# Performance work log

Hardware: AMD Instinct MI355X
Metric: run time of the kernel (lower is better)

Reference implementation:

```python
import jax, jax.numpy as jnp
import numpy as np

N_NODES = 100000
N_EDGES = 1600000
HID = 128
HEADS = 8
DK = HID // HEADS
N_LAYERS = 4
IN_DIM = 32
N_CLASSES = 16


def _ln(x, g, b, eps=1e-5):
    mu = x.mean(-1, keepdims=True)
    var = x.var(-1, keepdims=True)
    return (x - mu) / jnp.sqrt(var + eps) * g + b


def setup_inputs() -> dict:
    key = jax.random.key(0)
    ks = jax.random.split(key, 24)
    s = 0.05
    inp = {
        'feat': jax.random.randint(ks[0], (N_NODES,), 0, IN_DIM, dtype=jnp.int32),
        'edge_src': jax.random.randint(ks[1], (N_EDGES,), 0, N_NODES, dtype=jnp.int32),
        'edge_dst': jnp.sort(jax.random.randint(ks[2], (N_EDGES,), 0, N_NODES, dtype=jnp.int32)),
        'emb': jax.random.normal(ks[3], (IN_DIM, HID), jnp.float32) * s,
        'Wq': jax.random.normal(ks[4], (N_LAYERS, HID, HID), jnp.float32) * s,
        'Wk': jax.random.normal(ks[5], (N_LAYERS, HID, HID), jnp.float32) * s,
        'Wv': jax.random.normal(ks[6], (N_LAYERS, HID, HID), jnp.float32) * s,
        'Wo': jax.random.normal(ks[7], (N_LAYERS, HID, HID), jnp.float32) * s,
        'bo': jnp.zeros((N_LAYERS, HID), jnp.float32),
        'ln1_g': jnp.ones((N_LAYERS, HID), jnp.float32),
        'ln1_b': jnp.zeros((N_LAYERS, HID), jnp.float32),
        'W1': jax.random.normal(ks[8], (N_LAYERS, HID, 2 * HID), jnp.float32) * s,
        'b1': jnp.zeros((N_LAYERS, 2 * HID), jnp.float32),
        'W2': jax.random.normal(ks[9], (N_LAYERS, 2 * HID, HID), jnp.float32) * s,
        'b2': jnp.zeros((N_LAYERS, HID), jnp.float32),
        'ln2_g': jnp.ones((N_LAYERS, HID), jnp.float32),
        'ln2_b': jnp.zeros((N_LAYERS, HID), jnp.float32),
        'mW0': jax.random.normal(ks[10], (HID, HID // 2), jnp.float32) * s,
        'mb0': jnp.zeros((HID // 2,), jnp.float32),
        'mW1': jax.random.normal(ks[11], (HID // 2, HID // 4), jnp.float32) * s,
        'mb1': jnp.zeros((HID // 4,), jnp.float32),
        'mW2': jax.random.normal(ks[12], (HID // 4, N_CLASSES), jnp.float32) * s,
        'mb2': jnp.zeros((N_CLASSES,), jnp.float32),
    }
    return inp


def reference(feat, edge_src, edge_dst, emb, Wq, Wk, Wv, Wo, bo, ln1_g, ln1_b,
              W1, b1, W2, b2, ln2_g, ln2_b, mW0, mb0, mW1, mb1, mW2, mb2):
    N = feat.shape[0]
    h = emb[feat]  # [N, HID] embedding gather
    inv_sqrt_dk = jnp.float32(1.0 / np.sqrt(DK))
    for l in range(Wq.shape[0]):
        h_in1 = h
        q = (h @ Wq[l]).reshape(N, HEADS, DK)
        k = (h @ Wk[l]).reshape(N, HEADS, DK)
        v = (h @ Wv[l]).reshape(N, HEADS, DK)
        # per-edge scores: K[src] . Q[dst], scaled, clipped, exponentiated
        sc = jnp.einsum('ehd,ehd->eh', k[edge_src], q[edge_dst]) * inv_sqrt_dk
        sc = jnp.exp(jnp.clip(sc, -5.0, 5.0))  # [E, HEADS]
        wV = jax.ops.segment_sum(sc[:, :, None] * v[edge_src], edge_dst, num_segments=N)
        z = jax.ops.segment_sum(sc, edge_dst, num_segments=N)
        attn = (wV / (z[:, :, None] + 1e-6)).reshape(N, HID)
        h = h_in1 + (attn @ Wo[l] + bo[l])  # residual + O proj
        h = _ln(h, ln1_g[l], ln1_b[l])
        h_in2 = h
        f = jax.nn.relu(h @ W1[l] + b1[l]) @ W2[l] + b2[l]
        h = _ln(h_in2 + f, ln2_g[l], ln2_b[l])
    # MLPReadout: HID -> HID/2 -> HID/4 -> n_classes
    h = jax.nn.relu(h @ mW0 + mb0)
    h = jax.nn.relu(h @ mW1 + mb1)
    return h @ mW2 + mb2
```

## Files before the change

kernel.cpp:

```cpp
#include <hip/hip_runtime.h>
#include <hip/hip_fp16.h>

#define HID 128
#define N_LAYERS 4
#define IN_DIM 32
#define N_CLASSES 16

typedef _Float16 f16x8 __attribute__((ext_vector_type(8)));
typedef float f32x2 __attribute__((ext_vector_type(2)));
typedef __attribute__((ext_vector_type(4))) float f32x4;
typedef unsigned int uint_t;

#if defined(__has_builtin)
#if __has_builtin(__builtin_amdgcn_cvt_pk_f32_fp8)
#define HAVE_CVT_FP8 1
#endif
#if __has_builtin(__builtin_amdgcn_cvt_pk_fp8_f32)
#define HAVE_ENC_FP8 1
#endif
#endif

__device__ __forceinline__ unsigned short f2bf(float f) {
    unsigned int u = __float_as_uint(f);
    return (unsigned short)((u + 0x7FFFu + ((u >> 16) & 1u)) >> 16);
}
__device__ __forceinline__ float2 up16(uint_t u) {
    __half2 h = *(__half2*)&u;
    return __half22float2(h);
}

__device__ __forceinline__ unsigned char f2e4m3(float f) {
    unsigned int u = __float_as_uint(f);
    unsigned char s = (unsigned char)((u >> 24) & 0x80u);
    unsigned int a = u & 0x7FFFFFFFu;
    if (a >= 0x43E00000u) return s | 0x7Eu;
    int exp = (int)(a >> 23) - 127;
    if (exp < -6) {
        int m = (int)rintf(__uint_as_float(a) * 512.f);
        return s | (unsigned char)m;
    }
    unsigned int lsb = (a >> 20) & 1u;
    a += 0x7FFFFu + lsb;
    int e8 = ((int)(a >> 23) - 127) + 7;
    unsigned int m8 = (a >> 20) & 7u;
    return s | (unsigned char)((e8 << 3) | (int)m8);
}
__device__ __forceinline__ float e4m32f(unsigned int b) {
    unsigned int s = (b & 0x80u) << 24;
    unsigned int E = (b >> 3) & 15u, m = b & 7u;
    if (E == 0) {
        float v = (float)m * 0.001953125f;
        return __uint_as_float(__float_as_uint(v) | s);
    }
    return __uint_as_float(s | ((E + 120u) << 23) | (m << 20));
}
__device__ __forceinline__ unsigned char enc8(float v) {
#ifdef HAVE_ENC_FP8
    int r = __builtin_amdgcn_cvt_pk_fp8_f32(v, v, 0, false);
    return (unsigned char)(r & 0xFF);
#else
    return f2e4m3(v);
#endif
}
__device__ __forceinline__ void dec8v(uint_t u, f32x2* o) {
#ifdef HAVE_CVT_FP8
    o[0] = __builtin_amdgcn_cvt_pk_f32_fp8(u, false);
    o[1] = __builtin_amdgcn_cvt_pk_f32_fp8(u, true);
#else
    o[0] = (f32x2){e4m32f(u & 255u), e4m32f((u >> 8) & 255u)};
    o[1] = (f32x2){e4m32f((u >> 16) & 255u), e4m32f(u >> 24)};
#endif
}

__global__ void detect_kernel(const unsigned int* __restrict__ ln1g, int* __restrict__ flag) {
    if (threadIdx.x == 0 && blockIdx.x == 0)
        *flag = (ln1g[0] == 0x3F800000u) ? 0 : 1;
}

#define NSM 11
struct SArgs {
    const void* src[NSM];
    float*      dst[NSM];
    int         cnt[NSM];
};

__global__ void conv_kernel(SArgs args, const int* __restrict__ flag) {
    int p = blockIdx.y;
    int n = args.cnt[p];
    int base = (blockIdx.x * 256 + threadIdx.x) * 4;
    if (base >= n) return;
    float* dst = args.dst[p];
    if (*flag) {
        const unsigned short* s = (const unsigned short*)args.src[p];
        #pragma unroll
        for (int j = 0; j < 4; ++j)
            dst[base + j] = __uint_as_float(((unsigned int)s[base + j]) << 16);
    } else {
        const float* s = (const float*)args.src[p];
        *(float4*)&dst[base] = *(const float4*)&s[base];
    }
}

#define NW 27
struct WArgs {
    const void* src[NW];
    int         soff[NW];
    _Float16*   dst[NW];
    int         K[NW];
    int         M[NW];
};

__global__ void wconv_kernel(WArgs a, const int* __restrict__ flag) {
    int p = blockIdx.y;
    int K = a.K[p], M = a.M[p];
    int idx = blockIdx.x * 256 + threadIdx.x;
    if (idx >= K * M) return;
    int k = idx / M, m = idx % M;
    float v;
    if (*flag)
        v = __uint_as_float(((unsigned int)((const unsigned short*)a.src[p])[a.soff[p] + idx]) << 16);
    else
        v = ((const float*)a.src[p])[a.soff[p] + idx];
    a.dst[p][(size_t)m * K + k] = (_Float16)v;
}

__global__ void csr_kernel(const int* __restrict__ dst, int* __restrict__ row_start,
                           int N, int E) {
    int n = blockIdx.x * 256 + threadIdx.x;
    if (n > N) return;
    int lo = 0, hi = E;
    while (lo < hi) {
        int mid = (lo + hi) >> 1;
        if (dst[mid] < n) lo = mid + 1; else hi = mid;
    }
    row_start[n] = lo;
}

__global__ void embed_kernel(const int* __restrict__ feat, const float* __restrict__ emb,
                             _Float16* __restrict__ h, int N) {
    int idx = blockIdx.x * 256 + threadIdx.x;
    if (idx >= N * 16) return;
    int n  = idx >> 4;
    int c8 = idx & 15;
    int f = feat[n];
    const float* s = &emb[(size_t)f * HID + c8 * 8];
    float4 a = *(const float4*)s;
    float4 b = *(const float4*)(s + 4);
    f16x8 o;
    o[0] = (_Float16)a.x; o[1] = (_Float16)a.y; o[2] = (_Float16)a.z; o[3] = (_Float16)a.w;
    o[4] = (_Float16)b.x; o[5] = (_Float16)b.y; o[6] = (_Float16)b.z; o[7] = (_Float16)b.w;
    *(f16x8*)&h[(size_t)n * HID + c8 * 8] = o;
}

template<int K, int KC, int MC>
__launch_bounds__(256)
__global__ void mfma_gemm_qkv(const _Float16* __restrict__ Ain,
                              const _Float16* __restrict__ Bt,
                              _Float16* __restrict__ q16, unsigned char* __restrict__ kvp8) {
    constexpr int NT  = MC / 16;
    constexpr int SAB = KC * 2 + 16;

    __shared__ __align__(16) char As[64 * SAB];
    __shared__ __align__(16) char Bs[MC * SAB];

    const int t    = threadIdx.x;
    const int w    = t >> 6;
    const int l    = t & 63;
    const int quad = l >> 4;
    const int lc   = l & 15;
    const int row0 = blockIdx.x * 64;
    const int mbase = blockIdx.y * MC;

    f32x4 acc[NT];
    #pragma unroll
    for (int i = 0; i < NT; ++i) acc[i] = (f32x4){0.f, 0.f, 0.f, 0.f};

    {
        constexpr int AU = 64 * KC / 8;
        #pragma unroll
        for (int i = 0; i < (AU + 255) / 256; ++i) {
            int idx = t + i * 256;
            if ((AU % 256 == 0) || idx < AU) {
                int r = idx / (KC / 8), u = idx % (KC / 8);
                *(uint4*)&As[r * SAB + u * 16] =
                    *(const uint4*)(Ain + (size_t)(row0 + r) * K + u * 8);
            }
        }
        constexpr int BU = MC * KC / 8;
        #pragma unroll
        for (int i = 0; i < (BU + 255) / 256; ++i) {
            int idx = t + i * 256;
            if ((BU % 256 == 0) || idx < BU) {
                int m = idx / (KC / 8), u = idx % (KC / 8);
                *(uint4*)&Bs[m * SAB + u * 16] =
                    *(const uint4*)(Bt + (size_t)(mbase + m) * K + u * 8);
            }
        }
        __syncthreads();
        #pragma unroll
        for (int kk = 0; kk < KC / 32; ++kk) {
            f16x8 af = *(const f16x8*)&As[(w * 16 + lc) * SAB + kk * 64 + quad * 16];
            #pragma unroll
            for (int i = 0; i < NT; ++i) {
                f16x8 bf = *(const f16x8*)&Bs[(i * 16 + lc) * SAB + kk * 64 + quad * 16];
                acc[i] = __builtin_amdgcn_mfma_f32_16x16x32_f16(af, bf, acc[i], 0, 0, 0);
            }
        }
    }

    #pragma unroll
    for (int r = 0; r < 4; ++r) {
        int row = row0 + w * 16 + quad * 4 + r;
        #pragma unroll
        for (int i = 0; i < NT; ++i) {
            float v = acc[i][r];
            int gc = mbase + i * 16 + lc;
            if (gc < 128)      q16[(size_t)row * 128 + gc] = (_Float16)v;
            else if (gc < 256) kvp8[(size_t)row * 256 + (gc - 128)] = enc8(v);
            else               kvp8[(size_t)row * 256 + 128 + (gc - 256)] = enc8(v);
        }
    }
}

template<int NEXTM, bool RMODE>
__launch_bounds__(256)
__global__ void layer_tail_fused(const _Float16* __restrict__ t2, _Float16* __restrict__ h,
                                 const _Float16* __restrict__ Wo, const _Float16* __restrict__ W1,
                                 const _Float16* __restrict__ W2,
                                 const _Float16* __restrict__ Wn, const float* __restrict__ bn,
                                 const float* __restrict__ bo,  const float* __restrict__ l1g,
                                 const float* __restrict__ l1b, const float* __restrict__ b1,
                                 const float* __restrict__ b2,  const float* __restrict__ l2g,
                                 const float* __restrict__ l2b,
                                 _Float16* __restrict__ q16, unsigned char* __restrict__ kvp8) {
    constexpr int SAB = 272;
    __shared__ __align__(16) char bufA[64 * SAB];
    __shared__ __align__(16) char bufH[64 * SAB];
    __shared__ __align__(16) char bufB[64 * SAB];

    const int t = threadIdx.x, w = t >> 6, l = t & 63;
    const int quad = l >> 4, lc = l & 15;
    const int row0 = blockIdx.x * 64;
    const int arow = (w * 16 + lc) * SAB;

    _Float16 resv[4][8];
    #pragma unroll
    for (int r = 0; r < 4; ++r) {
        int row = row0 + w * 16 + quad * 4 + r;
        #pragma unroll
        for (int j = 0; j < 8; ++j)
            resv[r][j] = h[(size_t)row * 128 + j * 16 + lc];
    }

    #pragma unroll
    for (int i = 0; i < 4; ++i) {
        int idx = t + i * 256;
        int r = idx >> 4, u = idx & 15;
        *(uint4*)&bufA[r * SAB + u * 16] = *(const uint4*)(t2 + (size_t)(row0 + r) * 128 + u * 8);
    }

    auto stageW = [&](const _Float16* src, int rowStride) {
        __syncthreads();
        #pragma unroll
        for (int i = 0; i < 4; ++i) {
            int idx = t + i * 256;
            int r = idx >> 4, u = idx & 15;
            *(uint4*)&bufB[r * SAB + u * 16] =
                *(const uint4*)(src + (size_t)r * rowStride + u * 8);
        }
        __syncthreads();
    };
    auto mf4 = [&](const char* Ar, f32x4* acc) {
        #pragma unroll
        for (int kk = 0; kk < 4; ++kk) {
            f16x8 af = *(const f16x8*)(Ar + kk * 64 + quad * 16);
            #pragma unroll
            for (int i = 0; i < 4; ++i) {
                f16x8 bf = *(const f16x8*)&bufB[(i * 16 + lc) * SAB + kk * 64 + quad * 16];
                acc[i] = __builtin_amdgcn_mfma_f32_16x16x32_f16(af, bf, acc[i], 0, 0, 0);
            }
        }
    };

    f32x4 acc[8];
    #pragma unroll
    for (int i = 0; i < 8; ++i) acc[i] = (f32x4){0.f, 0.f, 0.f, 0.f};
    #pragma unroll
    for (int c = 0; c < 2; ++c) {
        stageW(Wo + (size_t)c * 64 * 128, 128);
        mf4(bufA + arow, acc + c * 4);
    }

    {
        float gv[8], bv[8], bb[8];
        #pragma unroll
        for (int j = 0; j < 8; ++j) {
            int col = j * 16 + lc;
            gv[j] = l1g[col]; bv[j] = l1b[col]; bb[j] = bo[col];
        }
        #pragma unroll
        for (int r = 0; r < 4; ++r) {
            int lrow = (w * 16 + quad * 4 + r) * SAB;
            float v[8];
            float s = 0.f, ss = 0.f;
            #pragma unroll
            for (int j = 0; j < 8; ++j) {
                v[j] = acc[j][r] + bb[j] + (float)resv[r][j];
                s += v[j]; ss += v[j] * v[j];
            }
            #pragma unroll
            for (int m = 1; m <= 8; m <<= 1) { s += __shfl_xor(s, m); ss += __shfl_xor(ss, m); }
            float mu   = s * (1.f / 128.f);
            float rstd = rsqrtf(ss * (1.f / 128.f) - mu * mu + 1e-5f);
            #pragma unroll
            for (int j = 0; j < 8; ++j) {
                float o = (v[j] - mu) * rstd * gv[j] + bv[j];
                *(_Float16*)&bufH[lrow + (j * 16 + lc) * 2] = (_Float16)o;
            }
        }
    }

    f32x4 acc3[8];
    #pragma unroll
    for (int i = 0; i < 8; ++i) acc3[i] = (f32x4){0.f, 0.f, 0.f, 0.f};
    #pragma unroll
    for (int half = 0; half < 2; ++half) {
        #pragma unroll
        for (int c2 = 0; c2 < 2; ++c2) {
            int c = half * 2 + c2;
            stageW(W1 + (size_t)c * 64 * 128, 128);
            f32x4 a2[4];
            #pragma unroll
            for (int i = 0; i < 4; ++i) a2[i] = (f32x4){0.f, 0.f, 0.f, 0.f};
            mf4(bufH + arow, a2);
            #pragma unroll
            for (int r = 0; r < 4; ++r) {
                int lrow = (w * 16 + quad * 4 + r) * SAB;
                #pragma unroll
                for (int i = 0; i < 4; ++i) {
                    float v = a2[i][r] + b1[c * 64 + i * 16 + lc];
                    v = fmaxf(v, 0.f);
                    *(_Float16*)&bufA[lrow + c2 * 128 + (i * 16 + lc) * 2] = (_Float16)v;
                }
            }
        }
        #pragma unroll
        for (int cc = 0; cc < 2; ++cc) {
            stageW(W2 + (size_t)cc * 64 * 256 + half * 128, 256);
            mf4(bufA + arow, acc3 + cc * 4);
        }
    }

    {
        float gv[8], bv[8], bb[8];
        #pragma unroll
        for (int j = 0; j < 8; ++j) {
            int col = j * 16 + lc;
            gv[j] = l2g[col]; bv[j] = l2b[col]; bb[j] = b2[col];
        }
        #pragma unroll
        for (int r = 0; r < 4; ++r) {
            int row = row0 + w * 16 + quad * 4 + r;
            int lrow = (w * 16 + quad * 4 + r) * SAB;
            float v[8];
            float s = 0.f, ss = 0.f;
            #pragma unroll
            for (int j = 0; j < 8; ++j) {
                float res = (float)*(const _Float16*)&bufH[lrow + (j * 16 + lc) * 2];
                v[j] = acc3[j][r] + bb[j] + res;
                s += v[j]; ss += v[j] * v[j];
            }
            #pragma unroll
            for (int m = 1; m <= 8; m <<= 1) { s += __shfl_xor(s, m); ss += __shfl_xor(ss, m); }
            float mu   = s * (1.f / 128.f);
            float rstd = rsqrtf(ss * (1.f / 128.f) - mu * mu + 1e-5f);
            #pragma unroll
            for (int j = 0; j < 8; ++j) {
                float o = (v[j] - mu) * rstd * gv[j] + bv[j];
                h[(size_t)row * 128 + j * 16 + lc] = (_Float16)o;
                *(_Float16*)&bufA[lrow + (j * 16 + lc) * 2] = (_Float16)o;
            }
        }
    }

    #pragma unroll
    for (int c = 0; c < NEXTM / 64; ++c) {
        stageW(Wn + (size_t)c * 64 * 128, 128);
        f32x4 a4[4];
        #pragma unroll
        for (int i = 0; i < 4; ++i) a4[i] = (f32x4){0.f, 0.f, 0.f, 0.f};
        mf4(bufA + arow, a4);
        #pragma unroll
        for (int r = 0; r < 4; ++r) {
            int row = row0 + w * 16 + quad * 4 + r;
            #pragma unroll
            for (int i = 0; i < 4; ++i) {
                int gc = c * 64 + i * 16 + lc;
                float v = a4[i][r];
                if (RMODE) {
                    v += bn[gc];
                    v = fmaxf(v, 0.f);
                    q16[(size_t)row * 64 + gc] = (_Float16)v;
                } else {
                    if (gc < 128)      q16[(size_t)row * 128 + gc] = (_Float16)v;
                    else if (gc < 256) kvp8[(size_t)row * 256 + (gc - 128)] = enc8(v);
                    else               kvp8[(size_t)row * 256 + 128 + (gc - 256)] = enc8(v);
                }
            }
        }
    }
}

__launch_bounds__(256)
__global__ void readout_tail(const _Float16* __restrict__ r0,
                             const _Float16* __restrict__ w1t, const float* __restrict__ b1_,
                             const _Float16* __restrict__ w2t, const float* __restrict__ b2_,
                             void* __restrict__ outp, const int* __restrict__ flag, int N) {
    constexpr int SA = 144;
    constexpr int SR = 80;
    __shared__ __align__(16) char bufA[64 * SA];
    __shared__ __align__(16) char bufR[64 * SR];

    const int t    = threadIdx.x;
    const int w    = t >> 6;
    const int l    = t & 63;
    const int quad = l >> 4;
    const int lc   = l & 15;
    const int row0 = blockIdx.x * 64;

    #pragma unroll
    for (int i = 0; i < 2; ++i) {
        int idx = t + i * 256;
        int r = idx >> 3, u = idx & 7;
        *(uint4*)&bufA[r * SA + u * 16] = *(const uint4*)(r0 + (size_t)(row0 + r) * 64 + u * 8);
    }
    __syncthreads();

    f32x4 acc[2];
    acc[0] = (f32x4){0.f, 0.f, 0.f, 0.f};
    acc[1] = (f32x4){0.f, 0.f, 0.f, 0.f};
    #pragma unroll
    for (int kk = 0; kk < 2; ++kk) {
        f16x8 af = *(const f16x8*)&bufA[(w * 16 + lc) * SA + kk * 64 + quad * 16];
        #pragma unroll
        for (int i = 0; i < 2; ++i) {
            f16x8 bf = *(const f16x8*)(w1t + (size_t)(i * 16 + lc) * 64 + kk * 32 + quad * 8);
            acc[i] = __builtin_amdgcn_mfma_f32_16x16x32_f16(af, bf, acc[i], 0, 0, 0);
        }
    }
    #pragma unroll
    for (int r = 0; r < 4; ++r) {
        int lrow = (w * 16 + quad * 4 + r) * SR;
        #pragma unroll
        for (int i = 0; i < 2; ++i) {
            float v = acc[i][r] + b1_[i * 16 + lc];
            v = fmaxf(v, 0.f);
            *(_Float16*)&bufR[lrow + (i * 16 + lc) * 2] = (_Float16)v;
        }
    }
    f32x4 a2 = (f32x4){0.f, 0.f, 0.f, 0.f};
    {
        f16x8 af = *(const f16x8*)&bufR[(w * 16 + lc) * SR + quad * 16];
        f16x8 bf = *(const f16x8*)(w2t + (size_t)lc * 32 + quad * 8);
        a2 = __builtin_amdgcn_mfma_f32_16x16x32_f16(af, bf, a2, 0, 0, 0);
    }
    #pragma unroll
    for (int r = 0; r < 4; ++r) {
        int row = row0 + w * 16 + quad * 4 + r;
        if (row < N) {
            float v = a2[r] + b2_[lc];
            size_t o = (size_t)row * 16 + lc;
            if (*flag) ((unsigned short*)outp)[o] = f2bf(v);
            else       ((float*)outp)[o] = v;
        }
    }
}

__global__ void attn_kernel(const _Float16* __restrict__ q16, const uint_t* __restrict__ kvp,
                            const int* __restrict__ esrc, const int* __restrict__ rows,
                            _Float16* __restrict__ out, int N) {
    int node = (blockIdx.x * blockDim.x + threadIdx.x) >> 6;
    if (node >= N) return;
    int l    = threadIdx.x & 63;
    int head = l & 7;
    int eg   = l >> 3;

    f32x2 qh[8];
    {
        const uint4* qp = (const uint4*)(q16 + (size_t)node * HID + head * 16);
        uint4 q0 = qp[0], q1 = qp[1];
        uint_t qs[8] = {q0.x, q0.y, q0.z, q0.w, q1.x, q1.y, q1.z, q1.w};
        #pragma unroll
        for (int i = 0; i < 8; ++i) {
            float2 f = up16(qs[i]);
            qh[i] = (f32x2){f.x * 0.25f, f.y * 0.25f};
        }
    }
    int e0 = rows[node], e1 = rows[node + 1];
    f32x2 wv[8];
    #pragma unroll
    for (int i = 0; i < 8; ++i) wv[i] = (f32x2){0.f, 0.f};
    float z = 0.f;

    for (int eb = e0; eb < e1; eb += 16) {
        int ea = eb + eg, ec = eb + 8 + eg;
        bool oka = ea < e1, okc = ec < e1;
        int sa  = esrc[oka ? ea : e1 - 1];
        int sc_ = esrc[okc ? ec : e1 - 1];
        uint4 ka = *(const uint4*)(kvp + (size_t)sa  * 64 + head * 4);
        uint4 va = *(const uint4*)(kvp + (size_t)sa  * 64 + 32 + head * 4);
        uint4 kc = *(const uint4*)(kvp + (size_t)sc_ * 64 + head * 4);
        uint4 vc = *(const uint4*)(kvp + (size_t)sc_ * 64 + 32 + head * 4);

        f32x2 k2a[8], k2c[8];
        dec8v(ka.x, k2a); dec8v(ka.y, k2a + 2); dec8v(ka.z, k2a + 4); dec8v(ka.w, k2a + 6);
        dec8v(kc.x, k2c); dec8v(kc.y, k2c + 2); dec8v(kc.z, k2c + 4); dec8v(kc.w, k2c + 6);
        f32x2 da2 = (f32x2){0.f, 0.f}, dc2 = (f32x2){0.f, 0.f};
        #pragma unroll
        for (int j = 0; j < 8; ++j) { da2 += qh[j] * k2a[j]; dc2 += qh[j] * k2c[j]; }
        float da = da2.x + da2.y, dc = dc2.x + dc2.y;
        float sa2 = oka ? __expf(fminf(fmaxf(da, -5.f), 5.f)) : 0.f;
        float sc2 = okc ? __expf(fminf(fmaxf(dc, -5.f), 5.f)) : 0.f;

        f32x2 v2a[8], v2c[8];
        dec8v(va.x, v2a); dec8v(va.y, v2a + 2); dec8v(va.z, v2a + 4); dec8v(va.w, v2a + 6);
        dec8v(vc.x, v2c); dec8v(vc.y, v2c + 2); dec8v(vc.z, v2c + 4); dec8v(vc.w, v2c + 6);
        f32x2 pa = (f32x2){sa2, sa2}, pc = (f32x2){sc2, sc2};
        #pragma unroll
        for (int j = 0; j < 8; ++j) { wv[j] += pa * v2a[j]; wv[j] += pc * v2c[j]; }
        z += sa2 + sc2;
    }
    #pragma unroll
    for (int m = 8; m < 64; m <<= 1) {
        z += __shfl_xor(z, m);
        #pragma unroll
        for (int i = 0; i < 8; ++i) {
            wv[i].x += __shfl_xor(wv[i].x, m);
            wv[i].y += __shfl_xor(wv[i].y, m);
        }
    }
    if (eg == 0) {
        float inv = 1.f / (z + 1e-6f);
        f16x8 o0, o1;
        #pragma unroll
        for (int i = 0; i < 4; ++i) {
            o0[2*i]   = (_Float16)(wv[i].x * inv);
            o0[2*i+1] = (_Float16)(wv[i].y * inv);
            o1[2*i]   = (_Float16)(wv[4+i].x * inv);
            o1[2*i+1] = (_Float16)(wv[4+i].y * inv);
        }
        *(f16x8*)&out[(size_t)node * HID + head * 16]     = o0;
        *(f16x8*)&out[(size_t)node * HID + head * 16 + 8] = o1;
    }
}

extern "C" void kernel_launch(void* const* d_in, const int* in_sizes, int n_in,
                              void* d_out, int out_size, void* d_ws, size_t ws_size,
                              hipStream_t stream) {
    const int N  = in_sizes[0];
    const int E  = in_sizes[1];
    const int RB = (N + 63) / 64;
    const size_t NP = (size_t)RB * 64;

    const int* d_feat = (const int*)d_in[0];
    const int* d_esrc = (const int*)d_in[1];
    const int* d_edst = (const int*)d_in[2];

    char* base = (char*)d_ws;
    size_t cur = 0;
    auto alloc = [&](size_t bytes) -> char* {
        cur = (cur + 255) & ~(size_t)255;
        char* p = base + cur;
        cur += bytes;
        return p;
    };
    int* d_flag = (int*)alloc(4);
    int* d_rows = (int*)alloc((size_t)(N + 1) * 4);

    float* p_emb = (float*)alloc(IN_DIM * HID * 4);
    float* p_bo  = (float*)alloc(N_LAYERS * HID * 4);
    float* p_l1g = (float*)alloc(N_LAYERS * HID * 4);
    float* p_l1b = (float*)alloc(N_LAYERS * HID * 4);
    float* p_b1  = (float*)alloc(N_LAYERS * 2 * HID * 4);
    float* p_b2  = (float*)alloc(N_LAYERS * HID * 4);
    float* p_l2g = (float*)alloc(N_LAYERS * HID * 4);
    float* p_l2b = (float*)alloc(N_LAYERS * HID * 4);
    float* p_mb0 = (float*)alloc(64 * 4);
    float* p_mb1 = (float*)alloc(32 * 4);
    float* p_mb2 = (float*)alloc(16 * 4);

    _Float16* wqkv_t = (_Float16*)alloc((size_t)N_LAYERS * 384 * 128 * 2);
    _Float16* wo_t   = (_Float16*)alloc((size_t)N_LAYERS * 128 * 128 * 2);
    _Float16* w1_t   = (_Float16*)alloc((size_t)N_LAYERS * 256 * 128 * 2);
    _Float16* w2_t   = (_Float16*)alloc((size_t)N_LAYERS * 128 * 256 * 2);
    _Float16* mw0_t  = (_Float16*)alloc(64 * 128 * 2);
    _Float16* mw1_t  = (_Float16*)alloc(32 * 64 * 2);
    _Float16* mw2_t  = (_Float16*)alloc(16 * 32 * 2);

    _Float16*      buf_h = (_Float16*)alloc(NP * HID * 2);
    _Float16*      q16   = (_Float16*)alloc(NP * HID * 2);
    _Float16*      t2    = (_Float16*)alloc(NP * HID * 2);
    unsigned char* kvp   = (unsigned char*)alloc(NP * 256);

    detect_kernel<<<1, 64, 0, stream>>>((const unsigned int*)d_in[9], d_flag);

    {
        SArgs sa;
        const int sidx[NSM] = {3, 8, 9, 10, 12, 14, 15, 16, 18, 20, 22};
        float*    sdst[NSM] = {p_emb, p_bo, p_l1g, p_l1b, p_b1, p_b2, p_l2g, p_l2b, p_mb0, p_mb1, p_mb2};
        const int scnt[NSM] = {IN_DIM*HID, N_LAYERS*HID, N_LAYERS*HID, N_LAYERS*HID,
                               N_LAYERS*2*HID, N_LAYERS*HID, N_LAYERS*HID, N_LAYERS*HID, 64, 32, 16};
        for (int i = 0; i < NSM; ++i) { sa.src[i] = d_in[sidx[i]]; sa.dst[i] = sdst[i]; sa.cnt[i] = scnt[i]; }
        conv_kernel<<<dim3(4, NSM), 256, 0, stream>>>(sa, d_flag);
    }

    {
        WArgs wa;
        int wi = 0;
        auto addw = [&](int inp, int off, int Kd, int Md, _Float16* dst) {
            wa.src[wi] = d_in[inp]; wa.soff[wi] = off; wa.K[wi] = Kd; wa.M[wi] = Md;
            wa.dst[wi] = dst; ++wi;
        };
        for (int l = 0; l < N_LAYERS; ++l) {
            addw(4,  l * 16384, 128, 128, wqkv_t + (size_t)l * 49152);
            addw(5,  l * 16384, 128, 128, wqkv_t + (size_t)l * 49152 + 16384);
            addw(6,  l * 16384, 128, 128, wqkv_t + (size_t)l * 49152 + 32768);
            addw(7,  l * 16384, 128, 128, wo_t + (size_t)l * 16384);
            addw(11, l * 32768, 128, 256, w1_t + (size_t)l * 32768);
            addw(13, l * 32768, 256, 128, w2_t + (size_t)l * 32768);
        }
        addw(17, 0, 128, 64, mw0_t);
        addw(19, 0, 64,  32, mw1_t);
        addw(21, 0, 32,  16, mw2_t);
        wconv_kernel<<<dim3(128, NW), 256, 0, stream>>>(wa, d_flag);
    }

    csr_kernel<<<(N + 1 + 255) / 256, 256, 0, stream>>>(d_edst, d_rows, N, E);
    embed_kernel<<<((size_t)N * 16 + 255) / 256, 256, 0, stream>>>(d_feat, p_emb, buf_h, N);

    const int GBW = (N + 3) / 4;

    mfma_gemm_qkv<128, 128, 192><<<dim3(RB, 2), 256, 0, stream>>>(buf_h, wqkv_t, q16, kvp);

    for (int l = 0; l < N_LAYERS; ++l) {
        const _Float16* Wo = wo_t + (size_t)l * 16384;
        const _Float16* W1 = w1_t + (size_t)l * 32768;
        const _Float16* W2 = w2_t + (size_t)l * 32768;
        const float* bo  = p_bo  + (size_t)l * HID;
        const float* l1g = p_l1g + (size_t)l * HID;
        const float* l1b = p_l1b + (size_t)l * HID;
        const float* b1  = p_b1  + (size_t)l * 2 * HID;
        const float* b2  = p_b2  + (size_t)l * HID;
        const float* l2g = p_l2g + (size_t)l * HID;
        const float* l2b = p_l2b + (size_t)l * HID;

        attn_kernel<<<GBW, 256, 0, stream>>>(q16, (const uint_t*)kvp, d_esrc, d_rows, t2, N);

        if (l < N_LAYERS - 1) {
            layer_tail_fused<384, false><<<RB, 256, 0, stream>>>(
                t2, buf_h, Wo, W1, W2, wqkv_t + (size_t)(l + 1) * 49152, nullptr,
                bo, l1g, l1b, b1, b2, l2g, l2b, q16, kvp);
        } else {
            layer_tail_fused<64, true><<<RB, 256, 0, stream>>>(
                t2, buf_h, Wo, W1, W2, mw0_t, p_mb0,
                bo, l1g, l1b, b1, b2, l2g, l2b, q16, nullptr);
        }
    }

    readout_tail<<<RB, 256, 0, stream>>>(q16, mw1_t, p_mb1, mw2_t, p_mb2, d_out, d_flag, N);
}
```

Baseline: 842.8 us.

## Read weight fragments directly from global memory in fused layer tail, drop shared staging

The fused per-layer tail kernel no longer stages weight tiles into a shared buffer with block-wide barriers. Each MFMA now loads its B fragments straight from global memory and relies on L1/L2 caching of the small weight matrices. Each wave also loads only its own rows of the input tile, so the syncs are removed. Dropping the third shared buffer and adding an occupancy hint of 4 blocks per SM is meant to raise concurrency, at the cost of more global and cache traffic per MFMA.

Measured after the change: 1.317 ms. 1.56x slower.

```diff
diff --git a/kernel.cpp b/kernel.cpp
--- a/kernel.cpp
+++ b/kernel.cpp
@@ -223,7 +223,7 @@
 }
 
 template<int NEXTM, bool RMODE>
-__launch_bounds__(256)
+__launch_bounds__(256, 4)
 __global__ void layer_tail_fused(const _Float16* __restrict__ t2, _Float16* __restrict__ h,
                                  const _Float16* __restrict__ Wo, const _Float16* __restrict__ W1,
                                  const _Float16* __restrict__ W2,
@@ -236,7 +236,6 @@
     constexpr int SAB = 272;
     __shared__ __align__(16) char bufA[64 * SAB];
     __shared__ __align__(16) char bufH[64 * SAB];
-    __shared__ __align__(16) char bufB[64 * SAB];
 
     const int t = threadIdx.x, w = t >> 6, l = t & 63;
     const int quad = l >> 4, lc = l & 15;
@@ -254,29 +253,19 @@
 
     #pragma unroll
     for (int i = 0; i < 4; ++i) {
-        int idx = t + i * 256;
+        int idx = l + i * 64;
         int r = idx >> 4, u = idx & 15;
-        *(uint4*)&bufA[r * SAB + u * 16] = *(const uint4*)(t2 + (size_t)(row0 + r) * 128 + u * 8);
-    }
-
-    auto stageW = [&](const _Float16* src, int rowStride) {
-        __syncthreads();
-        #pragma unroll
-        for (int i = 0; i < 4; ++i) {
-            int idx = t + i * 256;
-            int r = idx >> 4, u = idx & 15;
-            *(uint4*)&bufB[r * SAB + u * 16] =
-                *(const uint4*)(src + (size_t)r * rowStride + u * 8);
-        }
-        __syncthreads();
-    };
-    auto mf4 = [&](const char* Ar, f32x4* acc) {
+        *(uint4*)&bufA[(w * 16 + r) * SAB + u * 16] =
+            *(const uint4*)(t2 + (size_t)(row0 + w * 16 + r) * 128 + u * 8);
+    }
+
+    auto mf4g = [&](const char* Ar, const _Float16* B, int rs, f32x4* acc) {
         #pragma unroll
         for (int kk = 0; kk < 4; ++kk) {
             f16x8 af = *(const f16x8*)(Ar + kk * 64 + quad * 16);
             #pragma unroll
             for (int i = 0; i < 4; ++i) {
-                f16x8 bf = *(const f16x8*)&bufB[(i * 16 + lc) * SAB + kk * 64 + quad * 16];
+                f16x8 bf = *(const f16x8*)(B + (size_t)(i * 16 + lc) * rs + kk * 32 + quad * 8);
                 acc[i] = __builtin_amdgcn_mfma_f32_16x16x32_f16(af, bf, acc[i], 0, 0, 0);
             }
         }
@@ -286,10 +275,8 @@
     #pragma unroll
     for (int i = 0; i < 8; ++i) acc[i] = (f32x4){0.f, 0.f, 0.f, 0.f};
     #pragma unroll
-    for (int c = 0; c < 2; ++c) {
-        stageW(Wo + (size_t)c * 64 * 128, 128);
-        mf4(bufA + arow, acc + c * 4);
-    }
+    for (int c = 0; c < 2; ++c)
+        mf4g(bufA + arow, Wo + (size_t)c * 64 * 128, 128, acc + c * 4);
 
     {
         float gv[8], bv[8], bb[8];
@@ -328,11 +315,10 @@
         #pragma unroll
         for (int c2 = 0; c2 < 2; ++c2) {
             int c = half * 2 + c2;
-            stageW(W1 + (size_t)c * 64 * 128, 128);
             f32x4 a2[4];
             #pragma unroll
             for (int i = 0; i < 4; ++i) a2[i] = (f32x4){0.f, 0.f, 0.f, 0.f};
-            mf4(bufH + arow, a2);
+            mf4g(bufH + arow, W1 + (size_t)c * 64 * 128, 128, a2);
             #pragma unroll
             for (int r = 0; r < 4; ++r) {
                 int lrow = (w * 16 + quad * 4 + r) * SAB;
@@ -345,10 +331,8 @@
             }
         }
         #pragma unroll
-        for (int cc = 0; cc < 2; ++cc) {
-            stageW(W2 + (size_t)cc * 64 * 256 + half * 128, 256);
-            mf4(bufA + arow, acc3 + cc * 4);
-        }
+        for (int cc = 0; cc < 2; ++cc)
+            mf4g(bufA + arow, W2 + (size_t)cc * 64 * 256 + half * 128, 256, acc3 + cc * 4);
     }
 
     {
@@ -385,11 +369,10 @@
 
     #pragma unroll
     for (int c = 0; c < NEXTM / 64; ++c) {
-        stageW(Wn + (size_t)c * 64 * 128, 128);
         f32x4 a4[4];
         #pragma unroll
         for (int i = 0; i < 4; ++i) a4[i] = (f32x4){0.f, 0.f, 0.f, 0.f};
-        mf4(bufA + arow, a4);
+        mf4g(bufA + arow, Wn + (size_t)c * 64 * 128, 128, a4);
         #pragma unroll
         for (int r = 0; r < 4; ++r) {
             int row = row0 + w * 16 + quad * 4 + r;
```
